# Kernel tuning notes

Measured on AMD Instinct MI355X. Metric: run time of the kernel, lower is better.

Reference implementation:

```python
import jax, jax.numpy as jnp
import numpy as np

BLOCK_DIMS = (128, 256)
EPS = 1e-8


def l2norm(x, axis=-1):
    norm = jnp.sqrt(jnp.sum(x * x, axis=axis, keepdims=True)) + EPS
    return x / norm


def setup_inputs() -> dict:
    key = jax.random.key(0)
    k1, k2 = jax.random.split(key)
    img_emb = jax.random.normal(k1, (2048, 1024), dtype=jnp.float32)
    cap_emb = jax.random.normal(k2, (2048, 1024), dtype=jnp.float32)
    return {"img_emb": img_emb, "cap_emb": cap_emb}


def reference(img_emb, cap_emb):
    # Global l2norm of captions first (as in original forward)
    cap_emb = l2norm(cap_emb, -1)
    n_img, img_dim = img_emb.shape
    n_cap, cap_dim = cap_emb.shape
    sims = jnp.zeros((n_img, n_cap), dtype=img_emb.dtype)
    for block_dim in BLOCK_DIMS:
        v = img_dim // block_dim  # number of image blocks
        t = cap_dim // block_dim  # number of caption blocks
        # chunk along last dim + stack == reshape to [n, blocks, block_dim]
        img_blk = l2norm(img_emb.reshape(n_img, v, block_dim), -1)
        cap_blk = l2norm(cap_emb.reshape(n_cap, t, block_dim), -1)
        # [a, b, v, t] block-cosine similarities
        logits = jnp.einsum('avc,btc->abvt', img_blk, cap_blk)
        # max over image blocks v, then sum over caption blocks t
        sims = sims + jnp.max(logits, axis=2).sum(axis=-1)
    return sims
```

## Files before the change

kernel.cpp:

```cpp
#include <hip/hip_runtime.h>
#include <hip/hip_bf16.h>

typedef short short8 __attribute__((ext_vector_type(8)));
typedef float f32x4 __attribute__((ext_vector_type(4)));

#define EPSF 1e-8f
#define NROWS 16384

__device__ __forceinline__ unsigned short f2bf(float f) {
  __hip_bfloat16 h = __float2bfloat16(f);
  return *reinterpret_cast<unsigned short*>(&h);
}

template <int CTRL>
__device__ __forceinline__ float dmov(float x) {
  return __builtin_bit_cast(
      float, __builtin_amdgcn_mov_dpp(__builtin_bit_cast(int, x), CTRL, 0xF, 0xF, false));
}
#define DPP_XOR1 0xB1
#define DPP_XOR2 0x4E
#define DPP_P4 0x12C

__device__ __forceinline__ float swz16(float x) {
  return __builtin_bit_cast(
      float, __builtin_amdgcn_ds_swizzle(__builtin_bit_cast(int, x), 0x401F));
}

__global__ __launch_bounds__(256) void prep_kernel(
    const float* __restrict__ img, const float* __restrict__ cap,
    unsigned short* __restrict__ Ahat, unsigned short* __restrict__ Bhat,
    float* __restrict__ fa, float* __restrict__ fb)
{
  __shared__ float wsum[4];
  __shared__ uint2 lds2[16 * 18];
  int tid = threadIdx.x;
  int row = blockIdx.x & 2047;
  int isCap = blockIdx.x >> 11;
  const float* src = isCap ? cap : img;
  unsigned short* dstHat = isCap ? Bhat : Ahat;

  float4 v = reinterpret_cast<const float4*>(src + (size_t)row * 1024)[tid];
  float ss = v.x * v.x + v.y * v.y + v.z * v.z + v.w * v.w;
  ss += __shfl_xor(ss, 1);
  ss += __shfl_xor(ss, 2);
  ss += __shfl_xor(ss, 4);
  ss += __shfl_xor(ss, 8);
  ss += __shfl_xor(ss, 16);
  float s128 = ss;
  float s256 = s128 + __shfl_xor(s128, 32);

  if ((tid & 63) == 0) wsum[tid >> 6] = s256;
  __syncthreads();
  float rowsum = wsum[0] + wsum[1] + wsum[2] + wsum[3];
  float rn = sqrtf(rowsum) + EPSF;

  float scale;
  if (isCap) scale = 1.0f / (sqrtf(s128) + EPSF * rn);
  else       scale = 1.0f / (sqrtf(s128) + EPSF);

  unsigned int lo = (unsigned int)f2bf(v.x * scale) | ((unsigned int)f2bf(v.y * scale) << 16);
  unsigned int hi = (unsigned int)f2bf(v.z * scale) | ((unsigned int)f2bf(v.w * scale) << 16);

  int j = tid >> 5;
  int s = (tid & 31) >> 1;
  int half = tid & 1;
  lds2[s * 18 + j * 2 + half] = make_uint2(lo, hi);

  int l63 = tid & 63;
  if (l63 == 0 || l63 == 32) {
    float n128, n256;
    if (isCap) { n128 = sqrtf(s128) / rn + EPSF; n256 = sqrtf(s256) / rn + EPSF; }
    else       { n128 = sqrtf(s128) + EPSF;      n256 = sqrtf(s256) + EPSF; }
    float f = n128 / n256;
    int v256 = tid >> 6;
    float* dst = isCap ? fb : fa;
    dst[(row * 4 + v256) * 2 + (l63 == 32 ? 1 : 0)] = f;
  }
  __syncthreads();

  int s2 = tid >> 4, j2 = (tid & 15) >> 1, h2 = tid & 1;
  uint2 val = lds2[s2 * 18 + j2 * 2 + h2];
  *reinterpret_cast<uint2*>(
      (char*)dstHat + ((size_t)s2 * NROWS + row * 8 + j2) * 16 + h2 * 8) = val;
}

__global__ __launch_bounds__(256, 4) void sims_kernel(
    const unsigned short* __restrict__ Ahat, const unsigned short* __restrict__ Bhat,
    const float* __restrict__ fa, const float* __restrict__ fb,
    float* __restrict__ out)
{
  __shared__ float outLds[256];
  int tid = threadIdx.x;
  int lane = tid & 63;
  int w = tid >> 6;

  int bx = blockIdx.x;
  int x = bx & 7;
  int l = bx >> 3;
  int tm = l >> 4;
  int tn = (x << 4) | (l & 15);
  int m0 = tm * 128;
  int n0 = tn * 128;

  int wr = (w >> 1) * 64;
  int wc = (w & 1) * 64;
  int rl = lane & 15;
  int g = lane >> 4;

  unsigned vA = (unsigned)g * (NROWS * 16u) + (unsigned)(m0 + wr + rl) * 16u;
  unsigned vB = (unsigned)g * (NROWS * 16u) + (unsigned)(n0 + wc + rl) * 16u;
  const char* Abase = (const char*)Ahat;
  const char* Bbase = (const char*)Bhat;

  float2 fbv[4];
  int colBase = n0 + wc + rl;
#pragma unroll
  for (int fn = 0; fn < 4; ++fn)
    fbv[fn] = *reinterpret_cast<const float2*>(fb + ((colBase + fn * 16) >> 1) * 2);

  f32x4 acc[4][4] = {};

#pragma unroll
  for (int kt = 0; kt < 4; ++kt) {
    const char* Ak = Abase + (size_t)kt * (4u * NROWS * 16u);
    const char* Bk = Bbase + (size_t)kt * (4u * NROWS * 16u);
    short8 av[4], bv[4];
#pragma unroll
    for (int f = 0; f < 4; ++f) {
      av[f] = *reinterpret_cast<const short8*>(Ak + vA + f * 256);
      bv[f] = *reinterpret_cast<const short8*>(Bk + vB + f * 256);
    }
#pragma unroll
    for (int fm = 0; fm < 4; ++fm)
#pragma unroll
      for (int fn = 0; fn < 4; ++fn)
        acc[fm][fn] = __builtin_amdgcn_mfma_f32_16x16x32_bf16(av[fm], bv[fn], acc[fm][fn], 0, 0, 0);
  }

  bool writer = ((lane & 7) == 0) && ((g & 1) == 0);
  int pBase = ((wr >> 3) + (g >> 1)) * 16 + (wc >> 3) + (rl >> 3);

#pragma unroll
  for (int fm = 0; fm < 4; ++fm) {
    int rBase = m0 + wr + fm * 16 + 4 * g;
    int vi = rBase >> 1;
    float4 fav = *reinterpret_cast<const float4*>(fa + vi * 2);
#pragma unroll
    for (int fn = 0; fn < 4; ++fn) {
      f32x4 a = acc[fm][fn];

      float mm = fmaxf(fmaxf(a[0], a[1]), fmaxf(a[2], a[3]));
      float m8 = fmaxf(mm, swz16(mm));
      float u = m8 + dmov<DPP_XOR1>(m8);

      float s1 = dmov<DPP_XOR1>(a[1]);
      float s3 = dmov<DPP_XOR1>(a[3]);
      float qa = a[0] * (fav.x * fbv[fn].x) + s1 * (fav.y * fbv[fn].y);
      float qb = a[2] * (fav.z * fbv[fn].x) + s3 * (fav.w * fbv[fn].y);
      float qm = fmaxf(qa, qb);
      qm = fmaxf(qm, swz16(qm));

      float wv = u + qm;
      wv += dmov<DPP_XOR2>(wv);
      wv += dmov<DPP_P4>(wv);

      if (writer) outLds[pBase + fm * 32 + fn * 2] = wv;
    }
  }

  __syncthreads();
  int pr = tid >> 4, pc = tid & 15;
  out[(size_t)(tm * 16 + pr) * 2048 + (tn * 16 + pc)] = outLds[tid];
}

extern "C" void kernel_launch(void* const* d_in, const int* in_sizes, int n_in,
                              void* d_out, int out_size, void* d_ws, size_t ws_size,
                              hipStream_t stream) {
  const float* img = (const float*)d_in[0];
  const float* cap = (const float*)d_in[1];
  float* out = (float*)d_out;

  char* ws = (char*)d_ws;
  unsigned short* Ahat = (unsigned short*)ws;
  unsigned short* Bhat = (unsigned short*)(ws + (size_t)4 * 1024 * 1024);
  float* fa = (float*)(ws + (size_t)8 * 1024 * 1024);
  float* fb = fa + 2048 * 4 * 2;

  prep_kernel<<<4096, 256, 0, stream>>>(img, cap, Ahat, Bhat, fa, fb);
  sims_kernel<<<16384, 256, 0, stream>>>(Ahat, Bhat, fa, fb, out);
}
```

Baseline: 166.1 us.

## Widen sims tile to 128x256 per block and map prep rows to waves

The sims kernel now gives each wave all 128 rows of the A tile against 64 columns, so a block covers 128x256 output pairs. This halves the grid and lets each B fragment be reused across twice as many MFMAs, at the cost of double the accumulator registers, with launch bounds lowered to 2 blocks per SM to fit. The prep kernel now handles one row per wavefront using only shuffles, writing bf16 directly to the blocked layout without LDS or block barriers. That removes the shared-memory transpose and the syncs from prep.

```diff
diff --git a/kernel.cpp b/kernel.cpp
--- a/kernel.cpp
+++ b/kernel.cpp
@@ -31,65 +31,70 @@
     unsigned short* __restrict__ Ahat, unsigned short* __restrict__ Bhat,
     float* __restrict__ fa, float* __restrict__ fb)
 {
-  __shared__ float wsum[4];
-  __shared__ uint2 lds2[16 * 18];
   int tid = threadIdx.x;
-  int row = blockIdx.x & 2047;
-  int isCap = blockIdx.x >> 11;
-  const float* src = isCap ? cap : img;
+  int l = tid & 63;
+  int w = tid >> 6;
+  int rowid = blockIdx.x * 4 + w;
+  int isCap = rowid >> 11;
+  int row = rowid & 2047;
+  const float* src = (isCap ? cap : img) + (size_t)row * 1024;
   unsigned short* dstHat = isCap ? Bhat : Ahat;
 
-  float4 v = reinterpret_cast<const float4*>(src + (size_t)row * 1024)[tid];
-  float ss = v.x * v.x + v.y * v.y + v.z * v.z + v.w * v.w;
+  float4 v0 = reinterpret_cast<const float4*>(src)[l * 4 + 0];
+  float4 v1 = reinterpret_cast<const float4*>(src)[l * 4 + 1];
+  float4 v2 = reinterpret_cast<const float4*>(src)[l * 4 + 2];
+  float4 v3 = reinterpret_cast<const float4*>(src)[l * 4 + 3];
+
+  float ss = v0.x*v0.x + v0.y*v0.y + v0.z*v0.z + v0.w*v0.w
+           + v1.x*v1.x + v1.y*v1.y + v1.z*v1.z + v1.w*v1.w
+           + v2.x*v2.x + v2.y*v2.y + v2.z*v2.z + v2.w*v2.w
+           + v3.x*v3.x + v3.y*v3.y + v3.z*v3.z + v3.w*v3.w;
   ss += __shfl_xor(ss, 1);
   ss += __shfl_xor(ss, 2);
   ss += __shfl_xor(ss, 4);
-  ss += __shfl_xor(ss, 8);
-  ss += __shfl_xor(ss, 16);
   float s128 = ss;
-  float s256 = s128 + __shfl_xor(s128, 32);
-
-  if ((tid & 63) == 0) wsum[tid >> 6] = s256;
-  __syncthreads();
-  float rowsum = wsum[0] + wsum[1] + wsum[2] + wsum[3];
+  float s256 = s128 + __shfl_xor(s128, 8);
+  float s512 = s256 + __shfl_xor(s256, 16);
+  float rowsum = s512 + __shfl_xor(s512, 32);
   float rn = sqrtf(rowsum) + EPSF;
 
   float scale;
   if (isCap) scale = 1.0f / (sqrtf(s128) + EPSF * rn);
   else       scale = 1.0f / (sqrtf(s128) + EPSF);
 
-  unsigned int lo = (unsigned int)f2bf(v.x * scale) | ((unsigned int)f2bf(v.y * scale) << 16);
-  unsigned int hi = (unsigned int)f2bf(v.z * scale) | ((unsigned int)f2bf(v.w * scale) << 16);
+  unsigned int p0 = (unsigned)f2bf(v0.x*scale) | ((unsigned)f2bf(v0.y*scale) << 16);
+  unsigned int p1 = (unsigned)f2bf(v0.z*scale) | ((unsigned)f2bf(v0.w*scale) << 16);
+  unsigned int p2 = (unsigned)f2bf(v1.x*scale) | ((unsigned)f2bf(v1.y*scale) << 16);
+  unsigned int p3 = (unsigned)f2bf(v1.z*scale) | ((unsigned)f2bf(v1.w*scale) << 16);
+  unsigned int p4 = (unsigned)f2bf(v2.x*scale) | ((unsigned)f2bf(v2.y*scale) << 16);
+  unsigned int p5 = (unsigned)f2bf(v2.z*scale) | ((unsigned)f2bf(v2.w*scale) << 16);
+  unsigned int p6 = (unsigned)f2bf(v3.x*scale) | ((unsigned)f2bf(v3.y*scale) << 16);
+  unsigned int p7 = (unsigned)f2bf(v3.z*scale) | ((unsigned)f2bf(v3.w*scale) << 16);
 
-  int j = tid >> 5;
-  int s = (tid & 31) >> 1;
-  int half = tid & 1;
-  lds2[s * 18 + j * 2 + half] = make_uint2(lo, hi);
+  int rh = row * 8 + (l >> 3);
+  int s0 = (l & 7) * 2;
+  char* base = (char*)dstHat + ((size_t)s0 * NROWS + rh) * 16;
+  *reinterpret_cast<uint4*>(base) = make_uint4(p0, p1, p2, p3);
+  *reinterpret_cast<uint4*>(base + (size_t)NROWS * 16) = make_uint4(p4, p5, p6, p7);
 
-  int l63 = tid & 63;
-  if (l63 == 0 || l63 == 32) {
+  int l15 = l & 15;
+  if (l15 == 0 || l15 == 8) {
     float n128, n256;
     if (isCap) { n128 = sqrtf(s128) / rn + EPSF; n256 = sqrtf(s256) / rn + EPSF; }
     else       { n128 = sqrtf(s128) + EPSF;      n256 = sqrtf(s256) + EPSF; }
     float f = n128 / n256;
-    int v256 = tid >> 6;
+    int v256 = l >> 4;
     float* dst = isCap ? fb : fa;
-    dst[(row * 4 + v256) * 2 + (l63 == 32 ? 1 : 0)] = f;
+    dst[(row * 4 + v256) * 2 + (l15 >> 3)] = f;
   }
-  __syncthreads();
-
-  int s2 = tid >> 4, j2 = (tid & 15) >> 1, h2 = tid & 1;
-  uint2 val = lds2[s2 * 18 + j2 * 2 + h2];
-  *reinterpret_cast<uint2*>(
-      (char*)dstHat + ((size_t)s2 * NROWS + row * 8 + j2) * 16 + h2 * 8) = val;
 }
 
-__global__ __launch_bounds__(256, 4) void sims_kernel(
+__global__ __launch_bounds__(256, 2) void sims_kernel(
     const unsigned short* __restrict__ Ahat, const unsigned short* __restrict__ Bhat,
     const float* __restrict__ fa, const float* __restrict__ fb,
     float* __restrict__ out)
 {
-  __shared__ float outLds[256];
+  __shared__ float outLds[512];
   int tid = threadIdx.x;
   int lane = tid & 63;
   int w = tid >> 6;
@@ -97,17 +102,16 @@
   int bx = blockIdx.x;
   int x = bx & 7;
   int l = bx >> 3;
-  int tm = l >> 4;
-  int tn = (x << 4) | (l & 15);
+  int tm = l >> 3;
+  int tn = (x << 3) | (l & 7);
   int m0 = tm * 128;
-  int n0 = tn * 128;
+  int n0 = tn * 256;
 
-  int wr = (w >> 1) * 64;
-  int wc = (w & 1) * 64;
+  int wc = w * 64;
   int rl = lane & 15;
   int g = lane >> 4;
 
-  unsigned vA = (unsigned)g * (NROWS * 16u) + (unsigned)(m0 + wr + rl) * 16u;
+  unsigned vA = (unsigned)g * (NROWS * 16u) + (unsigned)(m0 + rl) * 16u;
   unsigned vB = (unsigned)g * (NROWS * 16u) + (unsigned)(n0 + wc + rl) * 16u;
   const char* Abase = (const char*)Ahat;
   const char* Bbase = (const char*)Bhat;
@@ -118,32 +122,32 @@
   for (int fn = 0; fn < 4; ++fn)
     fbv[fn] = *reinterpret_cast<const float2*>(fb + ((colBase + fn * 16) >> 1) * 2);
 
-  f32x4 acc[4][4] = {};
+  f32x4 acc[8][4] = {};
 
 #pragma unroll
   for (int kt = 0; kt < 4; ++kt) {
     const char* Ak = Abase + (size_t)kt * (4u * NROWS * 16u);
     const char* Bk = Bbase + (size_t)kt * (4u * NROWS * 16u);
-    short8 av[4], bv[4];
+    short8 av[8], bv[4];
 #pragma unroll
-    for (int f = 0; f < 4; ++f) {
+    for (int f = 0; f < 8; ++f)
       av[f] = *reinterpret_cast<const short8*>(Ak + vA + f * 256);
+#pragma unroll
+    for (int f = 0; f < 4; ++f)
       bv[f] = *reinterpret_cast<const short8*>(Bk + vB + f * 256);
-    }
 #pragma unroll
-    for (int fm = 0; fm < 4; ++fm)
+    for (int fm = 0; fm < 8; ++fm)
 #pragma unroll
       for (int fn = 0; fn < 4; ++fn)
         acc[fm][fn] = __builtin_amdgcn_mfma_f32_16x16x32_bf16(av[fm], bv[fn], acc[fm][fn], 0, 0, 0);
   }
 
   bool writer = ((lane & 7) == 0) && ((g & 1) == 0);
-  int pBase = ((wr >> 3) + (g >> 1)) * 16 + (wc >> 3) + (rl >> 3);
+  int pBase = (g >> 1) * 32 + (wc >> 3) + (rl >> 3);
 
 #pragma unroll
-  for (int fm = 0; fm < 4; ++fm) {
-    int rBase = m0 + wr + fm * 16 + 4 * g;
-    int vi = rBase >> 1;
+  for (int fm = 0; fm < 8; ++fm) {
+    int vi = (m0 + fm * 16 + 4 * g) >> 1;
     float4 fav = *reinterpret_cast<const float4*>(fa + vi * 2);
 #pragma unroll
     for (int fn = 0; fn < 4; ++fn) {
@@ -164,13 +168,17 @@
       wv += dmov<DPP_XOR2>(wv);
       wv += dmov<DPP_P4>(wv);
 
-      if (writer) outLds[pBase + fm * 32 + fn * 2] = wv;
+      if (writer) outLds[pBase + fm * 64 + fn * 2] = wv;
     }
   }
 
   __syncthreads();
-  int pr = tid >> 4, pc = tid & 15;
-  out[(size_t)(tm * 16 + pr) * 2048 + (tn * 16 + pc)] = outLds[tid];
+#pragma unroll
+  for (int i = 0; i < 2; ++i) {
+    int idx = tid + i * 256;
+    int pr = idx >> 5, pc = idx & 31;
+    out[(size_t)(tm * 16 + pr) * 2048 + (tn * 32 + pc)] = outLds[idx];
+  }
 }
 
 extern "C" void kernel_launch(void* const* d_in, const int* in_sizes, int n_in,
@@ -186,6 +194,6 @@
   float* fa = (float*)(ws + (size_t)8 * 1024 * 1024);
   float* fb = fa + 2048 * 4 * 2;
 
-  prep_kernel<<<4096, 256, 0, stream>>>(img, cap, Ahat, Bhat, fa, fb);
-  sims_kernel<<<16384, 256, 0, stream>>>(Ahat, Bhat, fa, fb, out);
+  prep_kernel<<<1024, 256, 0, stream>>>(img, cap, Ahat, Bhat, fa, fb);
+  sims_kernel<<<8192, 256, 0, stream>>>(Ahat, Bhat, fa, fb, out);
 }
```

After: 271.4 us. 1.63x slower.
